# Kernel optimization log

Hardware: AMD Instinct MI355X
Metric: run time of the kernel (lower is better)

The kernel has to match this reference:

```python
import jax, jax.numpy as jnp
import numpy as np
from jax import lax

DIM = 64
NUM_HEADS = 1
HEAD_DIM = DIM // NUM_HEADS
SR = 8  # reduction_ratio
SCALE = HEAD_DIM ** -0.5


def setup_inputs() -> dict:
    key = jax.random.key(0)
    ks = jax.random.split(key, 12)
    s = 0.02
    return {
        "x": jax.random.normal(ks[0], (8, 16384, DIM), dtype=jnp.float32),
        # conv sr: (out_ch, in_ch, kH, kW) torch OIHW layout
        "sr_w": jax.random.normal(ks[1], (DIM, DIM, SR, SR), dtype=jnp.float32) * s,
        "sr_b": jnp.zeros((DIM,), jnp.float32),
        "ln_g": jnp.ones((DIM,), jnp.float32),
        "ln_b": jnp.zeros((DIM,), jnp.float32),
        # torch Linear weights: (out_features, in_features)
        "q_w": jax.random.normal(ks[2], (DIM, DIM), dtype=jnp.float32) * s,
        "q_b": jnp.zeros((DIM,), jnp.float32),
        "kv_w": jax.random.normal(ks[3], (2 * DIM, DIM), dtype=jnp.float32) * s,
        "kv_b": jnp.zeros((2 * DIM,), jnp.float32),
        "proj_w": jax.random.normal(ks[4], (DIM, DIM), dtype=jnp.float32) * s,
        "proj_b": jnp.zeros((DIM,), jnp.float32),
    }


def _layernorm(x, g, b, eps=1e-5):
    mu = jnp.mean(x, axis=-1, keepdims=True)
    var = jnp.var(x, axis=-1, keepdims=True)
    return (x - mu) * lax.rsqrt(var + eps) * g + b


def reference(x, sr_w, sr_b, ln_g, ln_b, q_w, q_b, kv_w, kv_b, proj_w, proj_b):
    B, N, C = x.shape
    H = W = int(N ** 0.5)
    # q: (B, heads, N, head_dim)
    q = (x @ q_w.T + q_b).reshape(B, N, NUM_HEADS, HEAD_DIM).transpose(0, 2, 1, 3)
    # spatial reduction of KV via strided conv + LayerNorm
    x_ = x.transpose(0, 2, 1).reshape(B, C, H, W)
    x_ = lax.conv_general_dilated(
        x_, sr_w, window_strides=(SR, SR), padding="VALID",
        dimension_numbers=("NCHW", "OIHW", "NCHW"))
    x_ = x_ + sr_b[None, :, None, None]
    x_ = x_.reshape(B, C, -1).transpose(0, 2, 1)  # (B, Nr, C)
    x_ = _layernorm(x_, ln_g, ln_b)
    Nr = x_.shape[1]
    kv = (x_ @ kv_w.T + kv_b).reshape(B, Nr, 2, NUM_HEADS, HEAD_DIM)
    kv = kv.transpose(2, 0, 3, 1, 4)  # (2, B, heads, Nr, hd)
    k, v = kv[0], kv[1]
    attn = jnp.einsum("bhnd,bhmd->bhnm", q, k) * SCALE
    attn = jax.nn.softmax(attn, axis=-1)
    out = jnp.einsum("bhnm,bhmd->bhnd", attn, v)
    out = out.transpose(0, 2, 1, 3).reshape(B, N, C)
    return out @ proj_w.T + proj_b
```

## Files before the change

### kernel.cpp

```cpp
#include <hip/hip_runtime.h>
#include <hip/hip_bf16.h>


typedef __attribute__((ext_vector_type(8))) short bf16x8;
typedef __attribute__((ext_vector_type(4))) float f32x4;

__device__ __forceinline__ unsigned short f2bf(float f) {
    union { __hip_bfloat16 h; unsigned short u; } cv;
    cv.h = __hip_bfloat16(f);
    return cv.u;
}
union U8 { uint4 u; bf16x8 v; };
__device__ __forceinline__ bf16x8 pack8(float e0,float e1,float e2,float e3,
                                        float e4,float e5,float e6,float e7){
    U8 r;
    r.u.x = (unsigned)f2bf(e0) | ((unsigned)f2bf(e1)<<16);
    r.u.y = (unsigned)f2bf(e2) | ((unsigned)f2bf(e3)<<16);
    r.u.z = (unsigned)f2bf(e4) | ((unsigned)f2bf(e5)<<16);
    r.u.w = (unsigned)f2bf(e6) | ((unsigned)f2bf(e7)<<16);
    return r.v;
}
__device__ __forceinline__ bf16x8 ldg8(const unsigned short* p){
    U8 r; r.u = *(const uint4*)p; return r.v;
}

__global__ __launch_bounds__(256) void prep_kernel(
    const float* __restrict__ sr_w,
    const float* __restrict__ q_w, const float* __restrict__ q_b,
    const float* __restrict__ proj_w,
    unsigned short* __restrict__ wbp,
    unsigned short* __restrict__ qwb, unsigned short* __restrict__ pwp,
    float* __restrict__ qb_s)
{
    __shared__ float wsm[4096];
    int co = blockIdx.x;
    int t  = threadIdx.x;
    #pragma unroll
    for (int u = 0; u < 4; ++u) {
        int e = (u*256 + t)*4;
        *(float4*)&wsm[e] = *(const float4*)(sr_w + (size_t)co*4096 + e);
    }
    __syncthreads();
    int tc = co >> 4, n = co & 15;
    #pragma unroll
    for (int u = 0; u < 2; ++u) {
        int gidx = t*2 + u;
        int g = gidx & 3, j = (gidx>>2) & 15, kh = gidx >> 6;
        int kw = j >> 1, cinb = (j&1)*32 + 8*g;
        float e[8];
        #pragma unroll
        for (int i = 0; i < 8; ++i)
            e[i] = wsm[(cinb + i)*64 + kh*8 + kw];
        U8 tmp; tmp.v = pack8(e[0],e[1],e[2],e[3],e[4],e[5],e[6],e[7]);
        *(uint4*)(wbp + (size_t)((((kh*16 + j)*4 + tc)*4 + g)*16 + n)*8) = tmp.u;
    }
    int tid = co*256 + t;
    if (tid < 4096) qwb[tid] = f2bf(q_w[tid] * 0.125f);
    if (tid < 4096) {
        int i = tid & 7, g = (tid>>3)&3, s3 = (tid>>5)&1, co2 = tid>>6;
        int ch = 32*s3 + 16*(i>>2) + 4*g + (i&3);
        pwp[tid] = f2bf(proj_w[co2*64 + ch]);
    }
    if (tid < 64) qb_s[tid] = q_b[tid] * 0.125f;
}

__global__ __launch_bounds__(512) void convln_kernel(
    const float* __restrict__ x, const unsigned short* __restrict__ wbp,
    const float* __restrict__ sr_b,
    const float* __restrict__ ln_g, const float* __restrict__ ln_b,
    const float* __restrict__ kv_w, const float* __restrict__ kv_b,
    unsigned short* __restrict__ kbuf, unsigned short* __restrict__ vp)
{
    __shared__ char xsm[32768];
    int bid = blockIdx.x;
    int b = bid >> 6, oh = (bid >> 2) & 15, oq = bid & 3;
    int t = threadIdx.x;
    int w = t >> 6, lane = t & 63, g = lane >> 4, n = lane & 15;

    #pragma unroll
    for (int c2 = 0; c2 < 4; ++c2) {
        int eo = (c2*512 + t) * 8;
        int r = eo >> 11, inrow = eo & 2047;
        const float* src = x + ((size_t)((b*128 + oh*8 + r)*128 + oq*32))*64 + inrow;
        float4 v0 = *(const float4*)(src);
        float4 v1 = *(const float4*)(src + 4);
        U8 tmp; tmp.v = pack8(v0.x,v0.y,v0.z,v0.w,v1.x,v1.y,v1.z,v1.w);
        *(uint4*)(xsm + eo*2) = tmp.u;
    }
    __syncthreads();

    int pos = n & 3;
    f32x4 acc[4] = {{0,0,0,0},{0,0,0,0},{0,0,0,0},{0,0,0,0}};
    #pragma unroll
    for (int j = 0; j < 16; ++j) {
        int byte = ((w*32 + pos*8 + (j>>1))*64 + (j&1)*32 + 8*g) * 2;
        U8 Bx; Bx.u = *(const uint4*)(xsm + byte);
        #pragma unroll
        for (int tc = 0; tc < 4; ++tc) {
            bf16x8 A = ldg8(wbp + (size_t)((((w*16 + j)*4 + tc)*4 + g)*16 + n)*8);
            acc[tc] = __builtin_amdgcn_mfma_f32_16x16x32_bf16(A, Bx.v, acc[tc], 0, 0, 0);
        }
    }
    __syncthreads();

    float* red = (float*)xsm;
    float* ysp = (float*)(xsm + 8192);
    if (n < 4) {
        #pragma unroll
        for (int tc = 0; tc < 4; ++tc)
            *(f32x4*)(red + (w*4 + n)*64 + 16*tc + 4*g) = acc[tc];
    }
    __syncthreads();

    if (w < 4) {
        int p = w, c = lane;
        float val = sr_b[c];
        #pragma unroll
        for (int w8 = 0; w8 < 8; ++w8)
            val += red[(w8*4 + p)*64 + c];
        float s = val, s2 = val*val;
        #pragma unroll
        for (int o = 32; o >= 1; o >>= 1) {
            s  += __shfl_xor(s,  o, 64);
            s2 += __shfl_xor(s2, o, 64);
        }
        float mean = s * (1.f/64.f);
        float var  = s2 * (1.f/64.f) - mean*mean;
        float y = (val - mean) * rsqrtf(var + 1e-5f) * ln_g[c] + ln_b[c];
        ysp[p*64 + c] = y;
    }
    __syncthreads();
    if (w < 4) {
        int p = w, c = lane;
        int m = oh*16 + oq*4 + p;
        const float* yr = ysp + p*64;
        #pragma unroll
        for (int h = 0; h < 2; ++h) {
            int oc = c + h*64;
            float a2 = kv_b[oc];
            const float* wr = kv_w + oc*64;
            #pragma unroll
            for (int jj = 0; jj < 64; jj += 4) {
                float4 w4 = *(const float4*)(wr + jj);
                a2 += yr[jj]*w4.x + yr[jj+1]*w4.y + yr[jj+2]*w4.z + yr[jj+3]*w4.w;
            }
            if (h == 0) {
                kbuf[(b*256 + m)*64 + c] = f2bf(a2);
            } else {
                int ks2 = m >> 5, hi = (m >> 4) & 1, g2 = (m >> 2) & 3, r = m & 3;
                vp[(size_t)b*16384 + ((ks2*4 + g2)*64 + c)*8 + r + 4*hi] = f2bf(a2);
            }
        }
    }
}

__global__ __launch_bounds__(512) void attn_kernel(
    const float* __restrict__ x,
    const unsigned short* __restrict__ qwb, const float* __restrict__ qb_s,
    const unsigned short* __restrict__ kbuf, const unsigned short* __restrict__ vp,
    const unsigned short* __restrict__ pwp, const float* __restrict__ proj_b,
    float* __restrict__ out)
{
    __shared__ char Ks[32768];
    int bid = blockIdx.x;
    int b = bid >> 7, rt = bid & 127;
    int t = threadIdx.x;
    {
        const char* kb = (const char*)(kbuf + (size_t)b*16384);
        #pragma unroll
        for (int c = 0; c < 4; ++c) {
            int off = (c*512 + t) * 16;
            int dst = off ^ (((off >> 7) & 7) << 4);
            *(uint4*)(Ks + dst) = *(const uint4*)(kb + off);
        }
    }
    __syncthreads();

    int w = t >> 6, lane = t & 63, g = lane >> 4, n = lane & 15;
    int qrow = rt*128 + w*16 + n;
    const float* xr = x + ((size_t)b*16384 + qrow) * 64;
    const char* vpb = (const char*)(vp + (size_t)b*16384);

    f32x4 qacc[4];
    #pragma unroll
    for (int tau = 0; tau < 4; ++tau)
        qacc[tau] = *(const f32x4*)(qb_s + 16*tau + 4*g);
    bf16x8 xq[2];
    #pragma unroll
    for (int s = 0; s < 2; ++s) {
        float4 v0 = *(const float4*)(xr + 32*s + 8*g);
        float4 v1 = *(const float4*)(xr + 32*s + 8*g + 4);
        xq[s] = pack8(v0.x,v0.y,v0.z,v0.w,v1.x,v1.y,v1.z,v1.w);
    }
    #pragma unroll
    for (int tau = 0; tau < 4; ++tau)
        #pragma unroll
        for (int s = 0; s < 2; ++s) {
            bf16x8 A = ldg8(qwb + (16*tau + n)*64 + 32*s + 8*g);
            qacc[tau] = __builtin_amdgcn_mfma_f32_16x16x32_bf16(A, xq[s], qacc[tau], 0,0,0);
        }
    bf16x8 qkB[2];
    #pragma unroll
    for (int s2 = 0; s2 < 2; ++s2)
        qkB[s2] = pack8(qacc[2*s2][0],  qacc[2*s2][1],  qacc[2*s2][2],  qacc[2*s2][3],
                        qacc[2*s2+1][0],qacc[2*s2+1][1],qacc[2*s2+1][2],qacc[2*s2+1][3]);

    float S[16][4];
    #pragma unroll
    for (int tt = 0; tt < 16; ++tt) {
        f32x4 sa = {0.f, 0.f, 0.f, 0.f};
        int m = 16*tt + n;
        int base = m * 128;
        int swz = (m & 7) << 4;
        #pragma unroll
        for (int s2 = 0; s2 < 2; ++s2) {
            int c1 = (32*s2 + 4*g) * 2;
            uint2 d0 = *(const uint2*)(Ks + ((base + c1)      ^ swz));
            uint2 d1 = *(const uint2*)(Ks + ((base + c1 + 32) ^ swz));
            U8 A; A.u = make_uint4(d0.x, d0.y, d1.x, d1.y);
            sa = __builtin_amdgcn_mfma_f32_16x16x32_bf16(A.v, qkB[s2], sa, 0,0,0);
        }
        S[tt][0]=sa[0]; S[tt][1]=sa[1]; S[tt][2]=sa[2]; S[tt][3]=sa[3];
    }

    float rm[16];
    #pragma unroll
    for (int tt = 0; tt < 16; ++tt)
        rm[tt] = fmaxf(fmaxf(S[tt][0],S[tt][1]), fmaxf(S[tt][2],S[tt][3]));
    float m8[8];
    #pragma unroll
    for (int j = 0; j < 8; ++j) m8[j] = fmaxf(rm[2*j], rm[2*j+1]);
    float mx = fmaxf(fmaxf(fmaxf(m8[0],m8[1]),fmaxf(m8[2],m8[3])),
                     fmaxf(fmaxf(m8[4],m8[5]),fmaxf(m8[6],m8[7])));
    mx = fmaxf(mx, __shfl_xor(mx, 16, 64));
    mx = fmaxf(mx, __shfl_xor(mx, 32, 64));
    #pragma unroll
    for (int tt = 0; tt < 16; ++tt)
        #pragma unroll
        for (int r = 0; r < 4; ++r)
            S[tt][r] = __expf(S[tt][r] - mx);
    float rs[16];
    #pragma unroll
    for (int tt = 0; tt < 16; ++tt) rs[tt] = (S[tt][0]+S[tt][1]) + (S[tt][2]+S[tt][3]);
    float s8[8];
    #pragma unroll
    for (int j = 0; j < 8; ++j) s8[j] = rs[2*j] + rs[2*j+1];
    float ssum = ((s8[0]+s8[1])+(s8[2]+s8[3])) + ((s8[4]+s8[5])+(s8[6]+s8[7]));
    ssum += __shfl_xor(ssum, 16, 64);
    ssum += __shfl_xor(ssum, 32, 64);
    float inv = 1.f / ssum;

    f32x4 oacc[4] = {{0,0,0,0},{0,0,0,0},{0,0,0,0},{0,0,0,0}};
    #pragma unroll
    for (int ks = 0; ks < 8; ++ks) {
        bf16x8 Bp = pack8(S[2*ks][0],  S[2*ks][1],  S[2*ks][2],  S[2*ks][3],
                          S[2*ks+1][0],S[2*ks+1][1],S[2*ks+1][2],S[2*ks+1][3]);
        #pragma unroll
        for (int tc = 0; tc < 4; ++tc) {
            U8 A; A.u = *(const uint4*)(vpb + ((ks*4 + g)*64 + 16*tc + n) * 16);
            oacc[tc] = __builtin_amdgcn_mfma_f32_16x16x32_bf16(A.v, Bp, oacc[tc], 0,0,0);
        }
    }

    bf16x8 Bo[2];
    #pragma unroll
    for (int s3 = 0; s3 < 2; ++s3)
        Bo[s3] = pack8(oacc[2*s3][0]*inv,   oacc[2*s3][1]*inv,
                       oacc[2*s3][2]*inv,   oacc[2*s3][3]*inv,
                       oacc[2*s3+1][0]*inv, oacc[2*s3+1][1]*inv,
                       oacc[2*s3+1][2]*inv, oacc[2*s3+1][3]*inv);
    f32x4 pacc[4];
    #pragma unroll
    for (int tf = 0; tf < 4; ++tf)
        pacc[tf] = *(const f32x4*)(proj_b + 16*tf + 4*g);
    #pragma unroll
    for (int tf = 0; tf < 4; ++tf)
        #pragma unroll
        for (int s3 = 0; s3 < 2; ++s3) {
            bf16x8 Aw = ldg8(pwp + (((16*tf + n)*2 + s3)*4 + g)*8);
            pacc[tf] = __builtin_amdgcn_mfma_f32_16x16x32_bf16(Aw, Bo[s3], pacc[tf], 0,0,0);
        }
    float* orow = out + ((size_t)b*16384 + qrow) * 64;
    #pragma unroll
    for (int tf = 0; tf < 4; ++tf)
        *(float4*)(orow + 16*tf + 4*g) = *(float4*)&pacc[tf];
}

extern "C" void kernel_launch(void* const* d_in, const int* in_sizes, int n_in,
                              void* d_out, int out_size, void* d_ws, size_t ws_size,
                              hipStream_t stream)
{
    const float* x      = (const float*)d_in[0];
    const float* sr_w   = (const float*)d_in[1];
    const float* sr_b   = (const float*)d_in[2];
    const float* ln_g   = (const float*)d_in[3];
    const float* ln_b   = (const float*)d_in[4];
    const float* q_w    = (const float*)d_in[5];
    const float* q_b    = (const float*)d_in[6];
    const float* kv_w   = (const float*)d_in[7];
    const float* kv_b   = (const float*)d_in[8];
    const float* proj_w = (const float*)d_in[9];
    const float* proj_b = (const float*)d_in[10];
    float* out = (float*)d_out;

    char* wsb = (char*)d_ws;
    unsigned short* wbp  = (unsigned short*)(wsb);
    unsigned short* kbuf = (unsigned short*)(wsb + 524288);
    unsigned short* vp   = (unsigned short*)(wsb + 786432);
    unsigned short* qwb  = (unsigned short*)(wsb + 1048576);
    unsigned short* pwp  = (unsigned short*)(wsb + 1056768);
    float*          qb_s = (float*)(wsb + 1064960);

    hipLaunchKernelGGL(prep_kernel, dim3(64), dim3(256), 0, stream,
                       sr_w, q_w, q_b, proj_w, wbp, qwb, pwp, qb_s);
    hipLaunchKernelGGL(convln_kernel, dim3(512), dim3(512), 0, stream,
                       x, wbp, sr_b, ln_g, ln_b, kv_w, kv_b, kbuf, vp);
    hipLaunchKernelGGL(attn_kernel, dim3(1024), dim3(512), 0, stream,
                       x, qwb, qb_s, kbuf, vp, pwp, proj_b, out);
}
```

Baseline: 157.1 us.

## Stage x and output tiles through LDS for coalesced global access in attention

The attention kernel now loads the block's 128x64 fp32 x tile with fully coalesced float4 loads, converts it to bf16 and stores it swizzled in LDS, where each lane reads its MFMA fragment. The projected output is written to an LDS tile that reuses the K region and is then streamed out with coalesced float4 stores. The q weights are prepacked into fragment order so each lane issues one contiguous 16-byte load. This targets strided per-lane global accesses, at the cost of extra LDS (48KB, which may reduce occupancy) and two additional barriers.

```diff
diff --git a/kernel.cpp b/kernel.cpp
--- a/kernel.cpp
+++ b/kernel.cpp
@@ -29,7 +29,7 @@
     const float* __restrict__ q_w, const float* __restrict__ q_b,
     const float* __restrict__ proj_w,
     unsigned short* __restrict__ wbp,
-    unsigned short* __restrict__ qwb, unsigned short* __restrict__ pwp,
+    unsigned short* __restrict__ qwp, unsigned short* __restrict__ pwp,
     float* __restrict__ qb_s)
 {
     __shared__ float wsm[4096];
@@ -55,7 +55,10 @@
         *(uint4*)(wbp + (size_t)((((kh*16 + j)*4 + tc)*4 + g)*16 + n)*8) = tmp.u;
     }
     int tid = co*256 + t;
-    if (tid < 4096) qwb[tid] = f2bf(q_w[tid] * 0.125f);
+    if (tid < 4096) {
+        int i = tid & 7, n2 = (tid>>3)&15, g = (tid>>7)&3, s = (tid>>9)&1, tau = tid>>10;
+        qwp[tid] = f2bf(q_w[(16*tau + n2)*64 + 32*s + 8*g + i] * 0.125f);
+    }
     if (tid < 4096) {
         int i = tid & 7, g = (tid>>3)&3, s3 = (tid>>5)&1, co2 = tid>>6;
         int ch = 32*s3 + 16*(i>>2) + 4*g + (i&3);
@@ -156,15 +159,31 @@
 
 __global__ __launch_bounds__(512) void attn_kernel(
     const float* __restrict__ x,
-    const unsigned short* __restrict__ qwb, const float* __restrict__ qb_s,
+    const unsigned short* __restrict__ qwp, const float* __restrict__ qb_s,
     const unsigned short* __restrict__ kbuf, const unsigned short* __restrict__ vp,
     const unsigned short* __restrict__ pwp, const float* __restrict__ proj_b,
     float* __restrict__ out)
 {
-    __shared__ char Ks[32768];
+    __shared__ char sm[49152];
+    char* Xs = sm;
+    char* Ks = sm + 16384;
+    char* Outs = sm + 16384;
+
     int bid = blockIdx.x;
     int b = bid >> 7, rt = bid & 127;
     int t = threadIdx.x;
+    const size_t xelem = ((size_t)b*16384 + rt*128) * 64;
+
+    #pragma unroll
+    for (int c2 = 0; c2 < 4; ++c2) {
+        int elem = (c2*512 + t)*4;
+        int row = elem >> 6, col = elem & 63;
+        float4 v = *(const float4*)(x + xelem + elem);
+        unsigned lo = (unsigned)f2bf(v.x) | ((unsigned)f2bf(v.y)<<16);
+        unsigned hi = (unsigned)f2bf(v.z) | ((unsigned)f2bf(v.w)<<16);
+        uint2 pkt = make_uint2(lo, hi);
+        *(uint2*)(Xs + ((row*128 + col*2) ^ ((row&7)<<4))) = pkt;
+    }
     {
         const char* kb = (const char*)(kbuf + (size_t)b*16384);
         #pragma unroll
@@ -178,7 +197,7 @@
 
     int w = t >> 6, lane = t & 63, g = lane >> 4, n = lane & 15;
     int qrow = rt*128 + w*16 + n;
-    const float* xr = x + ((size_t)b*16384 + qrow) * 64;
+    int row16 = w*16 + n;
     const char* vpb = (const char*)(vp + (size_t)b*16384);
 
     f32x4 qacc[4];
@@ -188,15 +207,14 @@
     bf16x8 xq[2];
     #pragma unroll
     for (int s = 0; s < 2; ++s) {
-        float4 v0 = *(const float4*)(xr + 32*s + 8*g);
-        float4 v1 = *(const float4*)(xr + 32*s + 8*g + 4);
-        xq[s] = pack8(v0.x,v0.y,v0.z,v0.w,v1.x,v1.y,v1.z,v1.w);
+        U8 X; X.u = *(const uint4*)(Xs + ((row16*128 + 64*s + 16*g) ^ ((n&7)<<4)));
+        xq[s] = X.v;
     }
     #pragma unroll
     for (int tau = 0; tau < 4; ++tau)
         #pragma unroll
         for (int s = 0; s < 2; ++s) {
-            bf16x8 A = ldg8(qwb + (16*tau + n)*64 + 32*s + 8*g);
+            bf16x8 A = ldg8(qwp + (((tau*2 + s)*4 + g)*16 + n)*8);
             qacc[tau] = __builtin_amdgcn_mfma_f32_16x16x32_bf16(A, xq[s], qacc[tau], 0,0,0);
         }
     bf16x8 qkB[2];
@@ -222,6 +240,7 @@
         }
         S[tt][0]=sa[0]; S[tt][1]=sa[1]; S[tt][2]=sa[2]; S[tt][3]=sa[3];
     }
+    __syncthreads();
 
     float rm[16];
     #pragma unroll
@@ -280,10 +299,18 @@
             bf16x8 Aw = ldg8(pwp + (((16*tf + n)*2 + s3)*4 + g)*8);
             pacc[tf] = __builtin_amdgcn_mfma_f32_16x16x32_bf16(Aw, Bo[s3], pacc[tf], 0,0,0);
         }
-    float* orow = out + ((size_t)b*16384 + qrow) * 64;
+
     #pragma unroll
     for (int tf = 0; tf < 4; ++tf)
-        *(float4*)(orow + 16*tf + 4*g) = *(float4*)&pacc[tf];
+        *(f32x4*)(Outs + ((row16*256 + (16*tf + 4*g)*4) ^ ((n&7)<<4))) = pacc[tf];
+    __syncthreads();
+    #pragma unroll
+    for (int u = 0; u < 4; ++u) {
+        int elem = (u*512 + t)*4;
+        int row = elem >> 6, col = elem & 63;
+        f32x4 v = *(const f32x4*)(Outs + ((row*256 + col*4) ^ ((row&7)<<4)));
+        *(float4*)(out + xelem + elem) = *(float4*)&v;
+    }
 }
 
 extern "C" void kernel_launch(void* const* d_in, const int* in_sizes, int n_in,
@@ -307,14 +334,14 @@
     unsigned short* wbp  = (unsigned short*)(wsb);
     unsigned short* kbuf = (unsigned short*)(wsb + 524288);
     unsigned short* vp   = (unsigned short*)(wsb + 786432);
-    unsigned short* qwb  = (unsigned short*)(wsb + 1048576);
+    unsigned short* qwp  = (unsigned short*)(wsb + 1048576);
     unsigned short* pwp  = (unsigned short*)(wsb + 1056768);
     float*          qb_s = (float*)(wsb + 1064960);
 
     hipLaunchKernelGGL(prep_kernel, dim3(64), dim3(256), 0, stream,
-                       sr_w, q_w, q_b, proj_w, wbp, qwb, pwp, qb_s);
+                       sr_w, q_w, q_b, proj_w, wbp, qwp, pwp, qb_s);
     hipLaunchKernelGGL(convln_kernel, dim3(512), dim3(512), 0, stream,
                        x, wbp, sr_b, ln_g, ln_b, kv_w, kv_b, kbuf, vp);
     hipLaunchKernelGGL(attn_kernel, dim3(1024), dim3(512), 0, stream,
-                       x, qwb, qb_s, kbuf, vp, pwp, proj_b, out);
-}
+                       x, qwp, qb_s, kbuf, vp, pwp, proj_b, out);
+}
```

After: 157.2 us. No clear change (+0.1%).

## Halve attention block size, repack K smem for 16-byte reads, swizzle block order

Applied to the files above, without the earlier changes.

The attention kernel now runs 2048 blocks of 256 threads, each handling 64 query rows instead of 128. Blocks are remapped so consecutive block IDs interleave batches across XCDs. K is rearranged in shared memory so each MFMA operand is one 16-byte swizzled LDS read instead of two 8-byte reads. The q weights are prepacked into a lane-contiguous layout for coalesced loads, and s_setprio is raised around the MFMA loops. The cost is loading K into shared memory twice as often in total, since there are twice as many blocks.

```diff
diff --git a/kernel.cpp b/kernel.cpp
--- a/kernel.cpp
+++ b/kernel.cpp
@@ -29,7 +29,7 @@
     const float* __restrict__ q_w, const float* __restrict__ q_b,
     const float* __restrict__ proj_w,
     unsigned short* __restrict__ wbp,
-    unsigned short* __restrict__ qwb, unsigned short* __restrict__ pwp,
+    unsigned short* __restrict__ qwp, unsigned short* __restrict__ pwp,
     float* __restrict__ qb_s)
 {
     __shared__ float wsm[4096];
@@ -55,7 +55,10 @@
         *(uint4*)(wbp + (size_t)((((kh*16 + j)*4 + tc)*4 + g)*16 + n)*8) = tmp.u;
     }
     int tid = co*256 + t;
-    if (tid < 4096) qwb[tid] = f2bf(q_w[tid] * 0.125f);
+    if (tid < 4096) {
+        int i = tid & 7, n2 = (tid>>3)&15, g = (tid>>7)&3, s = (tid>>9)&1, tau = tid>>10;
+        qwp[tid] = f2bf(q_w[(16*tau + n2)*64 + 32*s + 8*g + i] * 0.125f);
+    }
     if (tid < 4096) {
         int i = tid & 7, g = (tid>>3)&3, s3 = (tid>>5)&1, co2 = tid>>6;
         int ch = 32*s3 + 16*(i>>2) + 4*g + (i&3);
@@ -154,30 +157,37 @@
     }
 }
 
-__global__ __launch_bounds__(512) void attn_kernel(
+__global__ __launch_bounds__(256) void attn_kernel(
     const float* __restrict__ x,
-    const unsigned short* __restrict__ qwb, const float* __restrict__ qb_s,
+    const unsigned short* __restrict__ qwp, const float* __restrict__ qb_s,
     const unsigned short* __restrict__ kbuf, const unsigned short* __restrict__ vp,
     const unsigned short* __restrict__ pwp, const float* __restrict__ proj_b,
     float* __restrict__ out)
 {
-    __shared__ char Ks[32768];
+    __shared__ uint4 KsV[2048];
     int bid = blockIdx.x;
-    int b = bid >> 7, rt = bid & 127;
+    int dbid = (bid & 7)*256 + (bid >> 3);
+    int b = dbid >> 8, rt = dbid & 255;
     int t = threadIdx.x;
+
     {
-        const char* kb = (const char*)(kbuf + (size_t)b*16384);
-        #pragma unroll
-        for (int c = 0; c < 4; ++c) {
-            int off = (c*512 + t) * 16;
-            int dst = off ^ (((off >> 7) & 7) << 4);
-            *(uint4*)(Ks + dst) = *(const uint4*)(kb + off);
+        const char* kb = (const char*)kbuf + (size_t)b*32768;
+        int m = t;
+        #pragma unroll
+        for (int s2 = 0; s2 < 2; ++s2) {
+            const uint4* src = (const uint4*)(kb + m*128 + s2*64);
+            uint4 L0 = src[0], L1 = src[1], L2 = src[2], L3 = src[3];
+            int base = m*8 + s2*4, sw = m & 7;
+            KsV[(base + 0) ^ sw] = make_uint4(L0.x, L0.y, L2.x, L2.y);
+            KsV[(base + 1) ^ sw] = make_uint4(L0.z, L0.w, L2.z, L2.w);
+            KsV[(base + 2) ^ sw] = make_uint4(L1.x, L1.y, L3.x, L3.y);
+            KsV[(base + 3) ^ sw] = make_uint4(L1.z, L1.w, L3.z, L3.w);
         }
     }
     __syncthreads();
 
     int w = t >> 6, lane = t & 63, g = lane >> 4, n = lane & 15;
-    int qrow = rt*128 + w*16 + n;
+    int qrow = rt*64 + w*16 + n;
     const float* xr = x + ((size_t)b*16384 + qrow) * 64;
     const char* vpb = (const char*)(vp + (size_t)b*16384);
 
@@ -196,7 +206,7 @@
     for (int tau = 0; tau < 4; ++tau)
         #pragma unroll
         for (int s = 0; s < 2; ++s) {
-            bf16x8 A = ldg8(qwb + (16*tau + n)*64 + 32*s + 8*g);
+            bf16x8 A = ldg8(qwp + (((tau*2 + s)*4 + g)*16 + n)*8);
             qacc[tau] = __builtin_amdgcn_mfma_f32_16x16x32_bf16(A, xq[s], qacc[tau], 0,0,0);
         }
     bf16x8 qkB[2];
@@ -206,22 +216,20 @@
                         qacc[2*s2+1][0],qacc[2*s2+1][1],qacc[2*s2+1][2],qacc[2*s2+1][3]);
 
     float S[16][4];
+    __builtin_amdgcn_s_setprio(1);
     #pragma unroll
     for (int tt = 0; tt < 16; ++tt) {
         f32x4 sa = {0.f, 0.f, 0.f, 0.f};
         int m = 16*tt + n;
-        int base = m * 128;
-        int swz = (m & 7) << 4;
+        int base = m*8, sw = m & 7;
         #pragma unroll
         for (int s2 = 0; s2 < 2; ++s2) {
-            int c1 = (32*s2 + 4*g) * 2;
-            uint2 d0 = *(const uint2*)(Ks + ((base + c1)      ^ swz));
-            uint2 d1 = *(const uint2*)(Ks + ((base + c1 + 32) ^ swz));
-            U8 A; A.u = make_uint4(d0.x, d0.y, d1.x, d1.y);
+            U8 A; A.u = KsV[(base + s2*4 + g) ^ sw];
             sa = __builtin_amdgcn_mfma_f32_16x16x32_bf16(A.v, qkB[s2], sa, 0,0,0);
         }
         S[tt][0]=sa[0]; S[tt][1]=sa[1]; S[tt][2]=sa[2]; S[tt][3]=sa[3];
     }
+    __builtin_amdgcn_s_setprio(0);
 
     float rm[16];
     #pragma unroll
@@ -251,6 +259,7 @@
     float inv = 1.f / ssum;
 
     f32x4 oacc[4] = {{0,0,0,0},{0,0,0,0},{0,0,0,0},{0,0,0,0}};
+    __builtin_amdgcn_s_setprio(1);
     #pragma unroll
     for (int ks = 0; ks < 8; ++ks) {
         bf16x8 Bp = pack8(S[2*ks][0],  S[2*ks][1],  S[2*ks][2],  S[2*ks][3],
@@ -261,6 +270,7 @@
             oacc[tc] = __builtin_amdgcn_mfma_f32_16x16x32_bf16(A.v, Bp, oacc[tc], 0,0,0);
         }
     }
+    __builtin_amdgcn_s_setprio(0);
 
     bf16x8 Bo[2];
     #pragma unroll
@@ -307,14 +317,14 @@
     unsigned short* wbp  = (unsigned short*)(wsb);
     unsigned short* kbuf = (unsigned short*)(wsb + 524288);
     unsigned short* vp   = (unsigned short*)(wsb + 786432);
-    unsigned short* qwb  = (unsigned short*)(wsb + 1048576);
+    unsigned short* qwp  = (unsigned short*)(wsb + 1048576);
     unsigned short* pwp  = (unsigned short*)(wsb + 1056768);
     float*          qb_s = (float*)(wsb + 1064960);
 
     hipLaunchKernelGGL(prep_kernel, dim3(64), dim3(256), 0, stream,
-                       sr_w, q_w, q_b, proj_w, wbp, qwb, pwp, qb_s);
+                       sr_w, q_w, q_b, proj_w, wbp, qwp, pwp, qb_s);
     hipLaunchKernelGGL(convln_kernel, dim3(512), dim3(512), 0, stream,
                        x, wbp, sr_b, ln_g, ln_b, kv_w, kv_b, kbuf, vp);
-    hipLaunchKernelGGL(attn_kernel, dim3(1024), dim3(512), 0, stream,
-                       x, qwb, qb_s, kbuf, vp, pwp, proj_b, out);
-}
+    hipLaunchKernelGGL(attn_kernel, dim3(2048), dim3(256), 0, stream,
+                       x, qwp, qb_s, kbuf, vp, pwp, proj_b, out);
+}
```

Measured after the change: 151.7 us. -3.5%, faster.
